# Kernel optimization log

Measured on AMD Instinct MI355X. Metric: run time of the kernel, lower is better.

## Reference

```python
import jax, jax.numpy as jnp
import numpy as np

B, L, K, H = 2, 2048, 48, 128
NUM_IN = 2 * H          # h_E (H) + gathered h_V (H)
SCALE = 30.0            # EncLayer scale
LN_EPS = 1e-5


def _linear_params(key, fan_in, fan_out):
    kw, kb = jax.random.split(key)
    s = 1.0 / np.sqrt(fan_in)
    W = jax.random.uniform(kw, (fan_in, fan_out), minval=-s, maxval=s, dtype=jnp.float32)
    b = jax.random.uniform(kb, (fan_out,), minval=-s, maxval=s, dtype=jnp.float32)
    return W, b


def setup_inputs() -> dict:
    key = jax.random.key(0)
    ks = jax.random.split(key, 12)
    h_V = jax.random.normal(ks[0], (B, L, H), dtype=jnp.float32)
    h_E = jax.random.normal(ks[1], (B, L, K, H), dtype=jnp.float32)
    E_idx = jax.random.randint(ks[2], (B, L, K), 0, L, dtype=jnp.int64)
    mask_V = jnp.ones((B, L), dtype=jnp.float32)
    mask_attend = jnp.ones((B, L, K), dtype=jnp.float32)

    W1, b1 = _linear_params(ks[3], H + NUM_IN, H)
    W2, b2 = _linear_params(ks[4], H, H)
    W3, b3 = _linear_params(ks[5], H, H)
    W11, b11 = _linear_params(ks[6], H + NUM_IN, H)
    W12, b12 = _linear_params(ks[7], H, H)
    W13, b13 = _linear_params(ks[8], H, H)
    Wi, bi = _linear_params(ks[9], H, 4 * H)   # PositionWiseFeedForward W_in
    Wo, bo = _linear_params(ks[10], 4 * H, H)  # W_out

    ln = lambda: (jnp.ones((H,), jnp.float32), jnp.zeros((H,), jnp.float32))
    ln1_s, ln1_b = ln(); ln2_s, ln2_b = ln(); ln3_s, ln3_b = ln()

    return dict(h_V=h_V, h_E=h_E, E_idx=E_idx, mask_V=mask_V, mask_attend=mask_attend,
                W1=W1, b1=b1, W2=W2, b2=b2, W3=W3, b3=b3,
                W11=W11, b11=b11, W12=W12, b12=b12, W13=W13, b13=b13,
                Wi=Wi, bi=bi, Wo=Wo, bo=bo,
                ln1_s=ln1_s, ln1_b=ln1_b, ln2_s=ln2_s, ln2_b=ln2_b,
                ln3_s=ln3_s, ln3_b=ln3_b)


def gather_nodes(nodes, idx):
    # nodes: [B, L, H], idx: [B, L, K] -> [B, L, K, H]
    b, l, h = nodes.shape
    flat = idx.reshape(b, -1)  # [B, L*K]
    g = jnp.take_along_axis(nodes, flat[..., None], axis=1)  # [B, L*K, H]
    return g.reshape(b, idx.shape[1], idx.shape[2], h)


def layer_norm(x, scale, bias):
    mu = jnp.mean(x, axis=-1, keepdims=True)
    var = jnp.mean((x - mu) ** 2, axis=-1, keepdims=True)
    return (x - mu) / jnp.sqrt(var + LN_EPS) * scale + bias


def gelu(x):
    return jax.nn.gelu(x, approximate=False)  # torch nn.GELU default (erf)


def enc_layer_forward(h_V, h_E, E_idx, mask_V, mask_attend, p):
    # --- node update: gather neighbors, concat, MLP, masked sum-reduce ---
    h_EV = jnp.concatenate([h_E, gather_nodes(h_V, E_idx)], axis=-1)        # [B,L,K,2H]
    h_V_exp = jnp.broadcast_to(h_V[:, :, None, :], h_EV.shape[:3] + (h_V.shape[-1],))
    h_EV = jnp.concatenate([h_V_exp, h_EV], axis=-1)                        # [B,L,K,3H]
    m = gelu(h_EV @ p['W1'] + p['b1'])
    m = gelu(m @ p['W2'] + p['b2'])
    m = m @ p['W3'] + p['b3']
    m = mask_attend[..., None] * m
    dh = jnp.sum(m, axis=-2) / SCALE                                        # [B,L,H]
    h_V = layer_norm(h_V + dh, p['ln1_s'], p['ln1_b'])
    # --- position-wise FFN ---
    dh = gelu(h_V @ p['Wi'] + p['bi']) @ p['Wo'] + p['bo']
    h_V = layer_norm(h_V + dh, p['ln2_s'], p['ln2_b'])
    h_V = mask_V[..., None] * h_V
    # --- edge update ---
    h_EV = jnp.concatenate([h_E, gather_nodes(h_V, E_idx)], axis=-1)
    h_V_exp = jnp.broadcast_to(h_V[:, :, None, :], h_EV.shape[:3] + (h_V.shape[-1],))
    h_EV = jnp.concatenate([h_V_exp, h_EV], axis=-1)
    m = gelu(h_EV @ p['W11'] + p['b11'])
    m = gelu(m @ p['W12'] + p['b12'])
    m = m @ p['W13'] + p['b13']
    h_E = layer_norm(h_E + m, p['ln3_s'], p['ln3_b'])
    return h_V, h_E


def reference(h_V, h_E, E_idx, mask_V, mask_attend,
              W1, b1, W2, b2, W3, b3, W11, b11, W12, b12, W13, b13,
              Wi, bi, Wo, bo, ln1_s, ln1_b, ln2_s, ln2_b, ln3_s, ln3_b):
    p = dict(W1=W1, b1=b1, W2=W2, b2=b2, W3=W3, b3=b3,
             W11=W11, b11=b11, W12=W12, b12=b12, W13=W13, b13=b13,
             Wi=Wi, bi=bi, Wo=Wo, bo=bo,
             ln1_s=ln1_s, ln1_b=ln1_b, ln2_s=ln2_s, ln2_b=ln2_b,
             ln3_s=ln3_s, ln3_b=ln3_b)
    return enc_layer_forward(h_V, h_E, E_idx, mask_V, mask_attend, p)
```

## Files before the change

kernel.cpp:

```cpp
#include <hip/hip_runtime.h>
#include <hip/hip_bf16.h>
#include <math.h>

typedef unsigned short u16;
typedef __attribute__((ext_vector_type(8))) short bf16x8;
typedef __attribute__((ext_vector_type(4))) float f32x4;
typedef __attribute__((ext_vector_type(4))) unsigned int uint4v;
typedef __attribute__((ext_vector_type(2))) unsigned int uint2v;
typedef __attribute__((ext_vector_type(4))) unsigned short u16x4;

#define BB 2
#define LL 2048
#define KN 48
#define HH 128
#define NBLK (BB*LL)
#define ST 136

#define WOFF      16
#define OFF_W1MT  (WOFF + 0)
#define OFF_W1ST  (WOFF + 16384)
#define OFF_W1GT  (WOFF + 32768)
#define OFF_W2T   (WOFF + 49152)
#define OFF_W3T   (WOFF + 65536)
#define OFF_W11MT (WOFF + 81920)
#define OFF_W11ST (WOFF + 98304)
#define OFF_W11GT (WOFF + 114688)
#define OFF_W12T  (WOFF + 131072)
#define OFF_W13T  (WOFF + 147456)
#define OFF_WIT   (WOFF + 163840)
#define OFF_WOT   (WOFF + 229376)
#define OFF_HV1   (WOFF + 294912)
#define OFF_Q1    (WOFF + 819200)
#define OFF_Q2    (WOFF + 1343488)
#define OFF_R1    (WOFF + 1867776)
#define OFF_R2    (WOFF + 2916352)
#define PREP_N    294912

__device__ __forceinline__ float b2f(u16 u){
    union { unsigned int i; float f; } v; v.i = ((unsigned int)u) << 16; return v.f;
}
__device__ __forceinline__ u16 f2b(float f){
    unsigned int x = __float_as_uint(f);
    unsigned int r = x + 0x7fffu + ((x >> 16) & 1u);
    return (u16)(r >> 16);
}
__device__ __forceinline__ unsigned int f2b2(float lo, float hi){
    unsigned int r;
    asm("v_cvt_pk_bf16_f32 %0, %1, %2" : "=v"(r) : "v"(lo), "v"(hi));
    return r;
}
__device__ __forceinline__ float gelu_f(float x){
    float ax = fabsf(x) * 0.70710678118654752f;
    float t  = __builtin_amdgcn_rcpf(fmaf(0.3275911f, ax, 1.0f));
    float e  = __builtin_amdgcn_exp2f(ax * ax * -1.4426950408889634f);
    float p  = fmaf(1.061405429f, t, -1.453152027f);
    p = fmaf(p, t, 1.421413741f);
    p = fmaf(p, t, -0.284496736f);
    p = fmaf(p, t, 0.254829592f);
    p = p * t;
    float erfv = fmaf(-p, e, 1.0f);
    float hx = 0.5f * x;
    return fmaf(fabsf(hx), erfv, hx);
}
__device__ __forceinline__ u16 ldb(const void* p, long i, int f32){
    return f32 ? f2b(((const float*)p)[i]) : ((const u16*)p)[i];
}
__device__ __forceinline__ float ldf(const void* p, long i, int f32){
    return f32 ? ((const float*)p)[i] : b2f(((const u16*)p)[i]);
}
__device__ __forceinline__ f32x4 ldf4(const void* p, long i, int f32){
    f32x4 r;
    if (f32){
        r = *(const f32x4*)((const float*)p + i);
    } else {
        u16x4 v = *(const u16x4*)((const u16*)p + i);
        r[0]=b2f(v[0]); r[1]=b2f(v[1]); r[2]=b2f(v[2]); r[3]=b2f(v[3]);
    }
    return r;
}
__device__ __forceinline__ void st4(void* p, long i, f32x4 v, int f32){
    if (f32){
        *(f32x4*)((float*)p + i) = v;
    } else {
        uint2v u; u.x = f2b2(v[0], v[1]); u.y = f2b2(v[2], v[3]);
        *(uint2v*)((u16*)p + i) = u;
    }
}
__device__ __forceinline__ void stage8(u16* dst, const void* src, long off, int f32){
    if (f32){
        const float* s = (const float*)src + off;
        f32x4 a = *(const f32x4*)(s);
        f32x4 b = *(const f32x4*)(s + 4);
        uint4v v;
        v.x = f2b2(a[0], a[1]); v.y = f2b2(a[2], a[3]);
        v.z = f2b2(b[0], b[1]); v.w = f2b2(b[2], b[3]);
        *(uint4v*)dst = v;
    } else {
        *(uint4v*)dst = *(const uint4v*)((const u16*)src + off);
    }
}
__device__ __forceinline__ int ld_idx(const void* p, int i, int i64){
    int v = i64 ? ((const int*)p)[2*i] : ((const int*)p)[i];
    return v & (LL - 1);
}

__global__ void prep_kernel(const void* W1, const void* W2, const void* W3,
                            const void* W11, const void* W12, const void* W13,
                            const void* Wi, const void* Wo,
                            const void* ln1s, const void* maskV, const void* eidx,
                            u16* wsbase){
    unsigned l0 = ((const unsigned*)ln1s)[0];
    unsigned m0 = ((const unsigned*)maskV)[0];
    const int f32 = (l0 == 0x3F800000u || m0 == 0x3F800000u) ? 1 : 0;
    if (blockIdx.x == 0 && threadIdx.x == 0){
        const int* e = (const int*)eidx;
        int orodd = 0, orlow = 0;
        for (int i = 1; i < 64; i += 2) orodd |= e[i];
        for (int i = 0; i < 64; i += 2) orlow |= e[i];
        ((int*)wsbase)[0] = f32;
        ((int*)wsbase)[1] = (orodd == 0 && orlow != 0) ? 1 : 0;
    }
    int i = blockIdx.x * 256 + threadIdx.x;
    if (i < 16384){ int n = i >> 7, k = i & 127; wsbase[OFF_W1MT + i] = ldb(W1, (128 + k)*128 + n, f32); }
    else if (i < 32768){ int j = i - 16384;  int n = j >> 7, k = j & 127; wsbase[OFF_W1ST  + j] = ldb(W1, k*128 + n, f32); }
    else if (i < 49152){ int j = i - 32768;  int n = j >> 7, k = j & 127; wsbase[OFF_W1GT  + j] = ldb(W1, (256 + k)*128 + n, f32); }
    else if (i < 65536){ int j = i - 49152;  int n = j >> 7, k = j & 127; wsbase[OFF_W2T   + j] = ldb(W2, k*128 + n, f32); }
    else if (i < 81920){ int j = i - 65536;  int n = j >> 7, k = j & 127; wsbase[OFF_W3T   + j] = ldb(W3, k*128 + n, f32); }
    else if (i < 98304){ int j = i - 81920;  int n = j >> 7, k = j & 127; wsbase[OFF_W11MT + j] = ldb(W11, (128 + k)*128 + n, f32); }
    else if (i < 114688){ int j = i - 98304; int n = j >> 7, k = j & 127; wsbase[OFF_W11ST + j] = ldb(W11, k*128 + n, f32); }
    else if (i < 131072){ int j = i - 114688;int n = j >> 7, k = j & 127; wsbase[OFF_W11GT + j] = ldb(W11, (256 + k)*128 + n, f32); }
    else if (i < 147456){ int j = i - 131072;int n = j >> 7, k = j & 127; wsbase[OFF_W12T  + j] = ldb(W12, k*128 + n, f32); }
    else if (i < 163840){ int j = i - 147456;int n = j >> 7, k = j & 127; wsbase[OFF_W13T  + j] = ldb(W13, k*128 + n, f32); }
    else if (i < 229376){ int j = i - 163840; int h = j >> 7, c = j & 127; wsbase[OFF_WIT + j] = ldb(Wi, c*512 + h, f32); }
    else if (i < 294912){ int j = i - 229376; int c = j >> 9, h = j & 511; wsbase[OFF_WOT + j] = ldb(Wo, h*128 + c, f32); }
}

__global__ __launch_bounds__(256) void precomp_kernel(
    const void* __restrict__ src, const void* __restrict__ bias,
    u16* __restrict__ wsbase, long offWs, long offWg, long offQ, long offR)
{
    __shared__ alignas(16) u16 X[16 * ST];
    const int f32 = ((const int*)wsbase)[0];
    const int t = threadIdx.x, lane = t & 63, w = t >> 6;
    const int node0 = blockIdx.x * 16;
    const int r16 = lane & 15, q = lane >> 4, q8 = q * 8;

    {
        int row = t >> 4, ch = t & 15;
        stage8(X + row * ST + ch * 8, src, ((long)(node0 + row)) * HH + ch * 8, f32);
    }
    __syncthreads();

    const u16* bp = X + r16 * ST + q8;
#pragma unroll
    for (int half = 0; half < 2; half++){
        long offW = half ? offWg : offWs;
#pragma unroll
        for (int nt = 0; nt < 2; nt++){
            int wr = w * 32 + nt * 16 + r16;
            const u16* ap = wsbase + offW + (long)wr * 128 + q8;
            f32x4 acc; acc[0]=0.f; acc[1]=0.f; acc[2]=0.f; acc[3]=0.f;
#pragma unroll
            for (int kk = 0; kk < 4; kk++){
                bf16x8 av = *(const bf16x8*)(ap + kk * 32);
                bf16x8 bv = *(const bf16x8*)(bp + kk * 32);
                acc = __builtin_amdgcn_mfma_f32_16x16x32_bf16(av, bv, acc, 0, 0, 0);
            }
            int c0 = w * 32 + nt * 16 + q * 4;
            if (half == 0){
                f32x4 bc = ldf4(bias, c0, f32);
                float* Rf = (float*)(wsbase + offR);
                f32x4 rr; rr[0]=acc[0]+bc[0]; rr[1]=acc[1]+bc[1]; rr[2]=acc[2]+bc[2]; rr[3]=acc[3]+bc[3];
                *(f32x4*)(Rf + (long)(node0 + r16) * HH + c0) = rr;
            } else {
                uint2v u; u.x = f2b2(acc[0], acc[1]); u.y = f2b2(acc[2], acc[3]);
                *(uint2v*)(wsbase + offQ + (long)(node0 + r16) * HH + c0) = u;
            }
        }
    }
}

__device__ __forceinline__ void mfma_WB(const u16* Mls, const bf16x8* W,
                                        f32x4 acc[3], int lane){
    const int r16 = lane & 15;
    const int q8  = (lane >> 4) * 8;
    const u16* bp = Mls + r16 * ST + q8;
#pragma unroll
    for (int kk = 0; kk < 4; kk++){
        bf16x8 b0 = *(const bf16x8*)(bp + kk * 32);
        bf16x8 b1 = *(const bf16x8*)(bp + 16 * ST + kk * 32);
        bf16x8 b2 = *(const bf16x8*)(bp + 32 * ST + kk * 32);
        acc[0] = __builtin_amdgcn_mfma_f32_16x16x32_bf16(W[kk], b0, acc[0], 0, 0, 0);
        acc[1] = __builtin_amdgcn_mfma_f32_16x16x32_bf16(W[kk], b1, acc[1], 0, 0, 0);
        acc[2] = __builtin_amdgcn_mfma_f32_16x16x32_bf16(W[kk], b2, acc[2], 0, 0, 0);
    }
}

__device__ __forceinline__ void zero_acc3(f32x4 acc[3]){
#pragma unroll
    for (int m = 0; m < 3; m++){ acc[m][0]=0.f; acc[m][1]=0.f; acc[m][2]=0.f; acc[m][3]=0.f; }
}

__device__ __forceinline__ void init_accT(f32x4 acc[3], const u16* Qg, int lane, int w){
    const int r16 = lane & 15, q = lane >> 4;
    const int c0 = w * 16 + q * 4;
#pragma unroll
    for (int mt = 0; mt < 3; mt++){
        u16x4 v = *(const u16x4*)(Qg + (mt * 16 + r16) * ST + c0);
        acc[mt][0]=b2f(v[0]); acc[mt][1]=b2f(v[1]); acc[mt][2]=b2f(v[2]); acc[mt][3]=b2f(v[3]);
    }
}

__device__ __forceinline__ void store_T(f32x4 acc[3], u16* M, f32x4 bc4,
                                        int lane, int w, bool dogelu){
    const int r16 = lane & 15, q = lane >> 4;
    const int c0 = w * 16 + q * 4;
#pragma unroll
    for (int mt = 0; mt < 3; mt++){
        float v0 = acc[mt][0] + bc4[0], v1 = acc[mt][1] + bc4[1];
        float v2 = acc[mt][2] + bc4[2], v3 = acc[mt][3] + bc4[3];
        if (dogelu){ v0 = gelu_f(v0); v1 = gelu_f(v1); v2 = gelu_f(v2); v3 = gelu_f(v3); }
        uint2v u; u.x = f2b2(v0, v1); u.y = f2b2(v2, v3);
        *(uint2v*)(M + (mt * 16 + r16) * ST + c0) = u;
    }
}

__global__ __launch_bounds__(512, 6) void node_kernel(
    const void* __restrict__ hV, const void* __restrict__ hE, const void* __restrict__ Eidx,
    const void* __restrict__ maskA,
    const void* __restrict__ b2, const void* __restrict__ b3,
    const void* __restrict__ ln1s, const void* __restrict__ ln1b,
    u16* __restrict__ wsbase)
{
    __shared__ alignas(16) u16 A[KN * ST];
    __shared__ alignas(16) u16 Qg[KN * ST];
    __shared__ float smask[KN];
    __shared__ alignas(16) float sL[HH];
    __shared__ alignas(16) float dh[HH];
    __shared__ float hv0f[HH];
    u16* M1 = Qg;

    const int f32 = ((const int*)wsbase)[0];
    const int i64 = ((const int*)wsbase)[1];
    const u16* ws = wsbase;
    const int t = threadIdx.x, lane = t & 63, w = t >> 6;
    const int bid = blockIdx.x;
    const int b = bid >> 11;
    const int r16 = lane & 15, q = lane >> 4, q8 = q * 8;
    const int wrow = w * 16 + r16;
    const int c0 = w * 16 + q * 4;

    bf16x8 B1[4];
    {
        const u16* bp = ws + OFF_W1MT + (long)wrow * 128 + q8;
#pragma unroll
        for (int k = 0; k < 4; k++) B1[k] = *(const bf16x8*)(bp + k * 32);
    }

    for (int i = t; i < 768; i += 512){
        int row = i >> 4, ch = i & 15;
        stage8(A + row * ST + ch * 8, hE, ((long)bid * KN + row) * HH + ch * 8, f32);
    }
    for (int i = t; i < 768; i += 512){
        int row = i >> 4, ch = i & 15;
        int nb = ld_idx(Eidx, bid * KN + row, i64);
        *(uint4v*)(Qg + row * ST + ch * 8) =
            *(const uint4v*)(ws + OFF_Q1 + ((long)b * LL + nb) * HH + ch * 8);
    }
    if (t < HH) hv0f[t] = ldf(hV, (long)bid * HH + t, f32);
    if (t < KN) smask[t] = ldf(maskA, bid * KN + t, f32);

    bf16x8 B2[4];
    {
        const u16* bp = ws + OFF_W2T + (long)wrow * 128 + q8;
#pragma unroll
        for (int k = 0; k < 4; k++) B2[k] = *(const bf16x8*)(bp + k * 32);
    }
    const f32x4 bc1 = *(const f32x4*)((const float*)(wsbase + OFF_R1) + (long)bid * HH + c0);
    __syncthreads();

    f32x4 acc[3];
    init_accT(acc, Qg, lane, w);
    __builtin_amdgcn_s_setprio(1);
    mfma_WB(A, B1, acc, lane);
    __builtin_amdgcn_s_setprio(0);
    store_T(acc, M1, bc1, lane, w, true);
    __syncthreads();

    zero_acc3(acc);
    __builtin_amdgcn_s_setprio(1);
    mfma_WB(M1, B2, acc, lane);
    __builtin_amdgcn_s_setprio(0);

    float cnt;
    {
        f32x4 b2v = ldf4(b2, c0, f32);
        f32x4 s; s[0]=0.f; s[1]=0.f; s[2]=0.f; s[3]=0.f;
        float cm = smask[r16] + smask[16 + r16] + smask[32 + r16];
#pragma unroll
        for (int mt = 0; mt < 3; mt++){
            float mk = smask[mt * 16 + r16];
#pragma unroll
            for (int j = 0; j < 4; j++)
                s[j] += mk * gelu_f(acc[mt][j] + b2v[j]);
        }
#pragma unroll
        for (int off = 1; off <= 8; off <<= 1){
#pragma unroll
            for (int j = 0; j < 4; j++) s[j] += __shfl_xor(s[j], off);
            cm += __shfl_xor(cm, off);
        }
        cnt = cm;
        if (r16 == 0) *(f32x4*)&sL[c0] = s;
    }
    __syncthreads();

    {
        int n = t >> 2, p = t & 3;
        const u16* wr = ws + OFF_W3T + (long)n * 128 + p * 32;
        float a = 0.f;
#pragma unroll
        for (int cc = 0; cc < 8; cc++){
            u16x4 wv = *(const u16x4*)(wr + cc * 4);
            f32x4 sv = *(const f32x4*)&sL[p * 32 + cc * 4];
            a = fmaf(b2f(wv[0]), sv[0], a);
            a = fmaf(b2f(wv[1]), sv[1], a);
            a = fmaf(b2f(wv[2]), sv[2], a);
            a = fmaf(b2f(wv[3]), sv[3], a);
        }
        a += __shfl_xor(a, 1);
        a += __shfl_xor(a, 2);
        if (p == 0) dh[n] = a + cnt * ldf(b3, n, f32);
    }
    __syncthreads();

    if (w == 0){
        float xa = hv0f[lane]      + dh[lane]      * (1.0f / 30.0f);
        float xb = hv0f[64 + lane] + dh[64 + lane] * (1.0f / 30.0f);
        float sum = xa + xb, sq = xa * xa + xb * xb;
#pragma unroll
        for (int off = 1; off < 64; off <<= 1){ sum += __shfl_xor(sum, off); sq += __shfl_xor(sq, off); }
        float mu = sum * (1.0f / 128.0f);
        float var = sq * (1.0f / 128.0f) - mu * mu;
        float rstd = rsqrtf(var + 1e-5f);
        wsbase[OFF_HV1 + (long)bid * HH + lane] =
            f2b((xa - mu) * rstd * ldf(ln1s, lane, f32) + ldf(ln1b, lane, f32));
        wsbase[OFF_HV1 + (long)bid * HH + 64 + lane] =
            f2b((xb - mu) * rstd * ldf(ln1s, 64 + lane, f32) + ldf(ln1b, 64 + lane, f32));
    }
}

__global__ __launch_bounds__(512, 6) void ffn_kernel(
    const void* __restrict__ maskV,
    const void* __restrict__ bi, const void* __restrict__ bo,
    const void* __restrict__ b11,
    const void* __restrict__ ln2s, const void* __restrict__ ln2b,
    u16* __restrict__ wsbase, void* __restrict__ dout)
{
    __shared__ alignas(16) u16 X[16 * 136];
    __shared__ alignas(16) u16 Hid[16 * 520];
    __shared__ alignas(16) float V[16 * 132];

    const int f32 = ((const int*)wsbase)[0];
    const u16* ws = wsbase;
    const u16* hv1 = wsbase + OFF_HV1;
    const int t = threadIdx.x, lane = t & 63, w = t >> 6;
    const int node0 = blockIdx.x * 16;
    const int r16 = lane & 15, q = lane >> 4, q8 = q * 8;
    const int c0 = w * 16 + q * 4;

    if (t < 256){
        int row = t >> 4, ch = t & 15;
        *(uint4v*)(X + row * 136 + ch * 8) =
            *(const uint4v*)(hv1 + (long)(node0 + row) * HH + ch * 8);
    }
    __syncthreads();

    f32x4 acc[4];
#pragma unroll
    for (int nt = 0; nt < 4; nt++){ acc[nt][0]=0.f; acc[nt][1]=0.f; acc[nt][2]=0.f; acc[nt][3]=0.f; }
    {
        const u16* bp = X + r16 * 136 + q8;
#pragma unroll
        for (int kk = 0; kk < 4; kk++){
            bf16x8 bv = *(const bf16x8*)(bp + kk * 32);
#pragma unroll
            for (int nt = 0; nt < 4; nt++){
                const u16* ap = ws + OFF_WIT + (long)(w * 64 + nt * 16 + r16) * 128 + kk * 32 + q8;
                bf16x8 av = *(const bf16x8*)ap;
                acc[nt] = __builtin_amdgcn_mfma_f32_16x16x32_bf16(av, bv, acc[nt], 0, 0, 0);
            }
        }
    }
#pragma unroll
    for (int nt = 0; nt < 4; nt++){
        int hc0 = w * 64 + nt * 16 + q * 4;
        f32x4 bc = ldf4(bi, hc0, f32);
        float g0 = gelu_f(acc[nt][0] + bc[0]), g1 = gelu_f(acc[nt][1] + bc[1]);
        float g2 = gelu_f(acc[nt][2] + bc[2]), g3 = gelu_f(acc[nt][3] + bc[3]);
        uint2v u; u.x = f2b2(g0, g1); u.y = f2b2(g2, g3);
        *(uint2v*)(Hid + r16 * 520 + hc0) = u;
    }
    __syncthreads();

    f32x4 acc2; acc2[0]=0.f; acc2[1]=0.f; acc2[2]=0.f; acc2[3]=0.f;
    {
        const u16* ap = ws + OFF_WOT + (long)(w * 16 + r16) * 512 + q8;
        const u16* bp = Hid + r16 * 520 + q8;
        __builtin_amdgcn_s_setprio(1);
#pragma unroll
        for (int kk = 0; kk < 16; kk++){
            bf16x8 av = *(const bf16x8*)(ap + kk * 32);
            bf16x8 bv = *(const bf16x8*)(bp + kk * 32);
            acc2 = __builtin_amdgcn_mfma_f32_16x16x32_bf16(av, bv, acc2, 0, 0, 0);
        }
        __builtin_amdgcn_s_setprio(0);
    }
    {
        f32x4 bo4 = ldf4(bo, c0, f32);
        u16x4 xr = *(const u16x4*)(X + r16 * 136 + c0);
        f32x4 vv;
        vv[0] = acc2[0] + bo4[0] + b2f(xr[0]);
        vv[1] = acc2[1] + bo4[1] + b2f(xr[1]);
        vv[2] = acc2[2] + bo4[2] + b2f(xr[2]);
        vv[3] = acc2[3] + bo4[3] + b2f(xr[3]);
        *(f32x4*)&V[r16 * 132 + c0] = vv;
    }
    __syncthreads();

    {
        int row = t >> 5, p = t & 31;
        f32x4 v = *(const f32x4*)&V[row * 132 + p * 4];
        float sum = v[0] + v[1] + v[2] + v[3];
        float sq = v[0]*v[0] + v[1]*v[1] + v[2]*v[2] + v[3]*v[3];
#pragma unroll
        for (int off = 1; off < 32; off <<= 1){ sum += __shfl_xor(sum, off); sq += __shfl_xor(sq, off); }
        float mu = sum * (1.0f / 128.0f);
        float var = sq * (1.0f / 128.0f) - mu * mu;
        float rstd = rsqrtf(var + 1e-5f);
        float mv = ldf(maskV, node0 + row, f32);
        f32x4 s4 = ldf4(ln2s, p * 4, f32), bb4 = ldf4(ln2b, p * 4, f32);
        f32x4 y;
#pragma unroll
        for (int j = 0; j < 4; j++) y[j] = ((v[j] - mu) * rstd * s4[j] + bb4[j]) * mv;
        st4(dout, (long)(node0 + row) * HH + p * 4, y, f32);
        uint2v u; u.x = f2b2(y[0], y[1]); u.y = f2b2(y[2], y[3]);
        *(uint2v*)(X + row * 136 + p * 4) = u;
    }
    __syncthreads();

    {
        const u16* bp = X + r16 * 136 + q8;
        f32x4 aR, aQ;
        aR[0]=0.f; aR[1]=0.f; aR[2]=0.f; aR[3]=0.f;
        aQ[0]=0.f; aQ[1]=0.f; aQ[2]=0.f; aQ[3]=0.f;
#pragma unroll
        for (int kk = 0; kk < 4; kk++){
            bf16x8 bv = *(const bf16x8*)(bp + kk * 32);
            bf16x8 avR = *(const bf16x8*)(ws + OFF_W11ST + (long)(w * 16 + r16) * 128 + kk * 32 + q8);
            bf16x8 avQ = *(const bf16x8*)(ws + OFF_W11GT + (long)(w * 16 + r16) * 128 + kk * 32 + q8);
            aR = __builtin_amdgcn_mfma_f32_16x16x32_bf16(avR, bv, aR, 0, 0, 0);
            aQ = __builtin_amdgcn_mfma_f32_16x16x32_bf16(avQ, bv, aQ, 0, 0, 0);
        }
        f32x4 b11v = ldf4(b11, c0, f32);
        float* Rf = (float*)(wsbase + OFF_R2);
        f32x4 rr;
#pragma unroll
        for (int j = 0; j < 4; j++) rr[j] = aR[j] + b11v[j];
        *(f32x4*)(Rf + (long)(node0 + r16) * HH + c0) = rr;
        uint2v u; u.x = f2b2(aQ[0], aQ[1]); u.y = f2b2(aQ[2], aQ[3]);
        *(uint2v*)(wsbase + OFF_Q2 + (long)(node0 + r16) * HH + c0) = u;
    }
}

__global__ __launch_bounds__(512, 6) void edge_kernel(
    const void* __restrict__ hE, const void* __restrict__ Eidx,
    const void* __restrict__ b12, const void* __restrict__ b13,
    const void* __restrict__ ln3s, const void* __restrict__ ln3b,
    u16* __restrict__ wsbase, void* __restrict__ dout)
{
    __shared__ alignas(16) u16 A[KN * ST];
    __shared__ alignas(16) u16 Qg[KN * ST];
    __shared__ float rowsum[KN];
    __shared__ float rowsq[KN];
    u16* M1 = Qg;
    u16* M2 = A;

    const int f32 = ((const int*)wsbase)[0];
    const int i64 = ((const int*)wsbase)[1];
    const u16* ws = wsbase;
    const int t = threadIdx.x, lane = t & 63, w = t >> 6;
    const int bid = blockIdx.x;
    const int b = bid >> 11;
    const int r16 = lane & 15, q = lane >> 4, q8 = q * 8;
    const int wrow = w * 16 + r16;
    const int c0 = w * 16 + q * 4;

    bf16x8 B1[4];
    {
        const u16* bp = ws + OFF_W11MT + (long)wrow * 128 + q8;
#pragma unroll
        for (int k = 0; k < 4; k++) B1[k] = *(const bf16x8*)(bp + k * 32);
    }

    for (int i = t; i < 768; i += 512){
        int row = i >> 4, ch = i & 15;
        stage8(A + row * ST + ch * 8, hE, ((long)bid * KN + row) * HH + ch * 8, f32);
    }
    for (int i = t; i < 768; i += 512){
        int row = i >> 4, ch = i & 15;
        int nb = ld_idx(Eidx, bid * KN + row, i64);
        *(uint4v*)(Qg + row * ST + ch * 8) =
            *(const uint4v*)(ws + OFF_Q2 + ((long)b * LL + nb) * HH + ch * 8);
    }
    if (t < KN){ rowsum[t] = 0.f; rowsq[t] = 0.f; }

    bf16x8 B2[4];
    {
        const u16* bp = ws + OFF_W12T + (long)wrow * 128 + q8;
#pragma unroll
        for (int k = 0; k < 4; k++) B2[k] = *(const bf16x8*)(bp + k * 32);
    }
    const f32x4 bc1 = *(const f32x4*)((const float*)(wsbase + OFF_R2) + (long)bid * HH + c0);
    __syncthreads();

    f32x4 acc[3];
    init_accT(acc, Qg, lane, w);
    __builtin_amdgcn_s_setprio(1);
    mfma_WB(A, B1, acc, lane);
    __builtin_amdgcn_s_setprio(0);
    store_T(acc, M1, bc1, lane, w, true);

    bf16x8 B3[4];
    {
        const u16* bp = ws + OFF_W13T + (long)wrow * 128 + q8;
#pragma unroll
        for (int k = 0; k < 4; k++) B3[k] = *(const bf16x8*)(bp + k * 32);
    }
    __syncthreads();

    zero_acc3(acc);
    __builtin_amdgcn_s_setprio(1);
    mfma_WB(M1, B2, acc, lane);
    __builtin_amdgcn_s_setprio(0);
    store_T(acc, M2, ldf4(b12, c0, f32), lane, w, true);
    __syncthreads();

    zero_acc3(acc);
    __builtin_amdgcn_s_setprio(1);
    mfma_WB(M2, B3, acc, lane);
    __builtin_amdgcn_s_setprio(0);

    f32x4 vals[3];
    {
        f32x4 b13v = ldf4(b13, c0, f32);
#pragma unroll
        for (int mt = 0; mt < 3; mt++){
            int r = mt * 16 + r16;
            f32x4 res = ldf4(hE, ((long)bid * KN + r) * HH + c0, f32);
#pragma unroll
            for (int j = 0; j < 4; j++) vals[mt][j] = acc[mt][j] + b13v[j] + res[j];
        }
    }
    {
        float s[3], ss[3];
#pragma unroll
        for (int mt = 0; mt < 3; mt++){
            s[mt]  = vals[mt][0] + vals[mt][1] + vals[mt][2] + vals[mt][3];
            ss[mt] = vals[mt][0]*vals[mt][0] + vals[mt][1]*vals[mt][1]
                   + vals[mt][2]*vals[mt][2] + vals[mt][3]*vals[mt][3];
            s[mt]  += __shfl_xor(s[mt], 16);  s[mt]  += __shfl_xor(s[mt], 32);
            ss[mt] += __shfl_xor(ss[mt], 16); ss[mt] += __shfl_xor(ss[mt], 32);
        }
        if (lane < 16){
#pragma unroll
            for (int mt = 0; mt < 3; mt++){
                atomicAdd(&rowsum[mt * 16 + lane], s[mt]);
                atomicAdd(&rowsq[mt * 16 + lane], ss[mt]);
            }
        }
    }
    __syncthreads();
    if (t < KN){
        float mu = rowsum[t] * (1.0f / 128.0f);
        float var = rowsq[t] * (1.0f / 128.0f) - mu * mu;
        rowsum[t] = mu;
        rowsq[t] = rsqrtf(var + 1e-5f);
    }
    __syncthreads();

    {
        long ebase = (long)BB * LL * HH;
        f32x4 g4 = ldf4(ln3s, c0, f32), be4 = ldf4(ln3b, c0, f32);
#pragma unroll
        for (int mt = 0; mt < 3; mt++){
            int r = mt * 16 + r16;
            float mu = rowsum[r], rs = rowsq[r];
            f32x4 y;
#pragma unroll
            for (int j = 0; j < 4; j++) y[j] = (vals[mt][j] - mu) * rs * g4[j] + be4[j];
            st4(dout, ebase + ((long)bid * KN + r) * HH + c0, y, f32);
        }
    }
}

extern "C" void kernel_launch(void* const* d_in, const int* in_sizes, int n_in,
                              void* d_out, int out_size, void* d_ws, size_t ws_size,
                              hipStream_t stream) {
    const void* hV    = d_in[0];
    const void* hE    = d_in[1];
    const void* Eidx  = d_in[2];
    const void* maskV = d_in[3];
    const void* maskA = d_in[4];
    const void* W1  = d_in[5];  const void* b1  = d_in[6];
    const void* W2  = d_in[7];  const void* b2  = d_in[8];
    const void* W3  = d_in[9];  const void* b3  = d_in[10];
    const void* W11 = d_in[11]; const void* b11 = d_in[12];
    const void* W12 = d_in[13]; const void* b12 = d_in[14];
    const void* W13 = d_in[15]; const void* b13 = d_in[16];
    const void* Wi  = d_in[17]; const void* bi  = d_in[18];
    const void* Wo  = d_in[19]; const void* bo  = d_in[20];
    const void* ln1s = d_in[21]; const void* ln1b = d_in[22];
    const void* ln2s = d_in[23]; const void* ln2b = d_in[24];
    const void* ln3s = d_in[25]; const void* ln3b = d_in[26];

    u16* ws = (u16*)d_ws;

    prep_kernel<<<(PREP_N + 255) / 256, 256, 0, stream>>>(W1, W2, W3, W11, W12, W13, Wi, Wo,
                                                          ln1s, maskV, Eidx, ws);
    precomp_kernel<<<NBLK / 16, 256, 0, stream>>>(hV, b1, ws,
                                                  (long)OFF_W1ST, (long)OFF_W1GT,
                                                  (long)OFF_Q1, (long)OFF_R1);
    node_kernel<<<NBLK, 512, 0, stream>>>(hV, hE, Eidx, maskA,
                                          b2, b3, ln1s, ln1b, ws);
    ffn_kernel<<<NBLK / 16, 512, 0, stream>>>(maskV, bi, bo, b11, ln2s, ln2b, ws, d_out);
    edge_kernel<<<NBLK, 512, 0, stream>>>(hE, Eidx, b12, b13,
                                          ln3s, ln3b, ws, d_out);
}
```

Before: 370.3 us.

## Process two nodes per block with register-prefetched next-node staging

Node and edge kernels now handle two consecutive nodes per block, launching half as many blocks. While the first node's MFMA chain runs, the second node's h_E tile and gathered Q rows are loaded into registers and written to a spare LDS buffer between barriers. This hides global load latency and amortizes the weight-fragment loads over two nodes. The cost is more LDS per block (an extra 48x136 tile), more live registers, and fewer blocks to fill the GPU, which may lower occupancy.

Result: slower. 576.8 us (+55.8%).

```diff
diff --git a/kernel.cpp b/kernel.cpp
--- a/kernel.cpp
+++ b/kernel.cpp
@@ -232,121 +232,168 @@
     const void* __restrict__ ln1s, const void* __restrict__ ln1b,
     u16* __restrict__ wsbase)
 {
-    __shared__ alignas(16) u16 A[KN * ST];
-    __shared__ alignas(16) u16 Qg[KN * ST];
-    __shared__ float smask[KN];
+    __shared__ alignas(16) u16 A0[KN * ST];
+    __shared__ alignas(16) u16 A1[KN * ST];
+    __shared__ alignas(16) u16 G[KN * ST];
+    __shared__ float smask2[2 * KN];
     __shared__ alignas(16) float sL[HH];
     __shared__ alignas(16) float dh[HH];
-    __shared__ float hv0f[HH];
-    u16* M1 = Qg;
+    __shared__ float hv0f2[2 * HH];
 
     const int f32 = ((const int*)wsbase)[0];
     const int i64 = ((const int*)wsbase)[1];
     const u16* ws = wsbase;
     const int t = threadIdx.x, lane = t & 63, w = t >> 6;
-    const int bid = blockIdx.x;
-    const int b = bid >> 11;
+    const int bid0 = blockIdx.x * 2;
     const int r16 = lane & 15, q = lane >> 4, q8 = q * 8;
     const int wrow = w * 16 + r16;
     const int c0 = w * 16 + q * 4;
 
-    bf16x8 B1[4];
+    bf16x8 B1[4], B2[4];
     {
         const u16* bp = ws + OFF_W1MT + (long)wrow * 128 + q8;
 #pragma unroll
         for (int k = 0; k < 4; k++) B1[k] = *(const bf16x8*)(bp + k * 32);
+        bp = ws + OFF_W2T + (long)wrow * 128 + q8;
+#pragma unroll
+        for (int k = 0; k < 4; k++) B2[k] = *(const bf16x8*)(bp + k * 32);
     }
 
     for (int i = t; i < 768; i += 512){
         int row = i >> 4, ch = i & 15;
-        stage8(A + row * ST + ch * 8, hE, ((long)bid * KN + row) * HH + ch * 8, f32);
-    }
-    for (int i = t; i < 768; i += 512){
-        int row = i >> 4, ch = i & 15;
-        int nb = ld_idx(Eidx, bid * KN + row, i64);
-        *(uint4v*)(Qg + row * ST + ch * 8) =
-            *(const uint4v*)(ws + OFF_Q1 + ((long)b * LL + nb) * HH + ch * 8);
-    }
-    if (t < HH) hv0f[t] = ldf(hV, (long)bid * HH + t, f32);
-    if (t < KN) smask[t] = ldf(maskA, bid * KN + t, f32);
-
-    bf16x8 B2[4];
-    {
-        const u16* bp = ws + OFF_W2T + (long)wrow * 128 + q8;
-#pragma unroll
-        for (int k = 0; k < 4; k++) B2[k] = *(const bf16x8*)(bp + k * 32);
-    }
-    const f32x4 bc1 = *(const f32x4*)((const float*)(wsbase + OFF_R1) + (long)bid * HH + c0);
+        stage8(A0 + row * ST + ch * 8, hE, ((long)bid0 * KN + row) * HH + ch * 8, f32);
+    }
+    {
+        const int b0 = bid0 >> 11;
+        for (int i = t; i < 768; i += 512){
+            int row = i >> 4, ch = i & 15;
+            int nb = ld_idx(Eidx, bid0 * KN + row, i64);
+            *(uint4v*)(G + row * ST + ch * 8) =
+                *(const uint4v*)(ws + OFF_Q1 + ((long)b0 * LL + nb) * HH + ch * 8);
+        }
+    }
+    if (t < 2 * HH) hv0f2[t] = ldf(hV, (long)bid0 * HH + t, f32);
+    if (t >= 416) smask2[t - 416] = ldf(maskA, (long)bid0 * KN + (t - 416), f32);
     __syncthreads();
 
-    f32x4 acc[3];
-    init_accT(acc, Qg, lane, w);
-    __builtin_amdgcn_s_setprio(1);
-    mfma_WB(A, B1, acc, lane);
-    __builtin_amdgcn_s_setprio(0);
-    store_T(acc, M1, bc1, lane, w, true);
-    __syncthreads();
-
-    zero_acc3(acc);
-    __builtin_amdgcn_s_setprio(1);
-    mfma_WB(M1, B2, acc, lane);
-    __builtin_amdgcn_s_setprio(0);
-
-    float cnt;
-    {
-        f32x4 b2v = ldf4(b2, c0, f32);
-        f32x4 s; s[0]=0.f; s[1]=0.f; s[2]=0.f; s[3]=0.f;
-        float cm = smask[r16] + smask[16 + r16] + smask[32 + r16];
-#pragma unroll
-        for (int mt = 0; mt < 3; mt++){
-            float mk = smask[mt * 16 + r16];
-#pragma unroll
-            for (int j = 0; j < 4; j++)
-                s[j] += mk * gelu_f(acc[mt][j] + b2v[j]);
-        }
-#pragma unroll
-        for (int off = 1; off <= 8; off <<= 1){
-#pragma unroll
-            for (int j = 0; j < 4; j++) s[j] += __shfl_xor(s[j], off);
-            cm += __shfl_xor(cm, off);
-        }
-        cnt = cm;
-        if (r16 == 0) *(f32x4*)&sL[c0] = s;
-    }
-    __syncthreads();
-
-    {
-        int n = t >> 2, p = t & 3;
-        const u16* wr = ws + OFF_W3T + (long)n * 128 + p * 32;
-        float a = 0.f;
-#pragma unroll
-        for (int cc = 0; cc < 8; cc++){
-            u16x4 wv = *(const u16x4*)(wr + cc * 4);
-            f32x4 sv = *(const f32x4*)&sL[p * 32 + cc * 4];
-            a = fmaf(b2f(wv[0]), sv[0], a);
-            a = fmaf(b2f(wv[1]), sv[1], a);
-            a = fmaf(b2f(wv[2]), sv[2], a);
-            a = fmaf(b2f(wv[3]), sv[3], a);
-        }
-        a += __shfl_xor(a, 1);
-        a += __shfl_xor(a, 2);
-        if (p == 0) dh[n] = a + cnt * ldf(b3, n, f32);
-    }
-    __syncthreads();
-
-    if (w == 0){
-        float xa = hv0f[lane]      + dh[lane]      * (1.0f / 30.0f);
-        float xb = hv0f[64 + lane] + dh[64 + lane] * (1.0f / 30.0f);
-        float sum = xa + xb, sq = xa * xa + xb * xb;
-#pragma unroll
-        for (int off = 1; off < 64; off <<= 1){ sum += __shfl_xor(sum, off); sq += __shfl_xor(sq, off); }
-        float mu = sum * (1.0f / 128.0f);
-        float var = sq * (1.0f / 128.0f) - mu * mu;
-        float rstd = rsqrtf(var + 1e-5f);
-        wsbase[OFF_HV1 + (long)bid * HH + lane] =
-            f2b((xa - mu) * rstd * ldf(ln1s, lane, f32) + ldf(ln1b, lane, f32));
-        wsbase[OFF_HV1 + (long)bid * HH + 64 + lane] =
-            f2b((xb - mu) * rstd * ldf(ln1s, 64 + lane, f32) + ldf(ln1b, 64 + lane, f32));
+    f32x4 hf0, hf1, hf2; uint4v hb0, hb1, qg0, qg1;
+
+    for (int j = 0; j < 2; ++j){
+        const int n = bid0 + j;
+        u16* Ac = j ? A1 : A0;
+        u16* An = j ? A0 : A1;
+        const f32x4 bc1 = *(const f32x4*)((const float*)(wsbase + OFF_R1) + (long)n * HH + c0);
+
+        if (j == 0){
+            const int n1 = bid0 + 1;
+            const int bn1 = n1 >> 11;
+            if (f32){
+                const float* s = (const float*)hE + (long)n1 * KN * HH;
+                hf0 = *(const f32x4*)(s + t * 4);
+                hf1 = *(const f32x4*)(s + (t + 512) * 4);
+                hf2 = *(const f32x4*)(s + (t + 1024) * 4);
+            } else {
+                const u16* s = (const u16*)hE + (long)n1 * KN * HH;
+                hb0 = *(const uint4v*)(s + t * 8);
+                if (t < 256) hb1 = *(const uint4v*)(s + (t + 512) * 8);
+            }
+            {
+                int nb = ld_idx(Eidx, n1 * KN + (t >> 4), i64);
+                qg0 = *(const uint4v*)(ws + OFF_Q1 + ((long)bn1 * LL + nb) * HH + (t & 15) * 8);
+                if (t < 256){
+                    int nb1 = ld_idx(Eidx, n1 * KN + ((512 + t) >> 4), i64);
+                    qg1 = *(const uint4v*)(ws + OFF_Q1 + ((long)bn1 * LL + nb1) * HH + ((512 + t) & 15) * 8);
+                }
+            }
+        }
+
+        f32x4 acc[3];
+        init_accT(acc, G, lane, w);
+        __builtin_amdgcn_s_setprio(1);
+        mfma_WB(Ac, B1, acc, lane);
+        __builtin_amdgcn_s_setprio(0);
+        store_T(acc, G, bc1, lane, w, true);
+        __syncthreads();
+
+        zero_acc3(acc);
+        __builtin_amdgcn_s_setprio(1);
+        mfma_WB(G, B2, acc, lane);
+        __builtin_amdgcn_s_setprio(0);
+
+        float cnt;
+        {
+            f32x4 b2v = ldf4(b2, c0, f32);
+            f32x4 s; s[0]=0.f; s[1]=0.f; s[2]=0.f; s[3]=0.f;
+            float cm = smask2[j*KN + r16] + smask2[j*KN + 16 + r16] + smask2[j*KN + 32 + r16];
+#pragma unroll
+            for (int mt = 0; mt < 3; mt++){
+                float mk = smask2[j*KN + mt * 16 + r16];
+#pragma unroll
+                for (int jj = 0; jj < 4; jj++)
+                    s[jj] += mk * gelu_f(acc[mt][jj] + b2v[jj]);
+            }
+#pragma unroll
+            for (int off = 1; off <= 8; off <<= 1){
+#pragma unroll
+                for (int jj = 0; jj < 4; jj++) s[jj] += __shfl_xor(s[jj], off);
+                cm += __shfl_xor(cm, off);
+            }
+            cnt = cm;
+            if (r16 == 0) *(f32x4*)&sL[c0] = s;
+        }
+        if (j == 0){
+            if (f32){
+                uint2v u;
+                u.x = f2b2(hf0[0], hf0[1]); u.y = f2b2(hf0[2], hf0[3]);
+                *(uint2v*)(An + (t >> 5) * ST + (t & 31) * 4) = u;
+                u.x = f2b2(hf1[0], hf1[1]); u.y = f2b2(hf1[2], hf1[3]);
+                *(uint2v*)(An + ((t + 512) >> 5) * ST + ((t + 512) & 31) * 4) = u;
+                u.x = f2b2(hf2[0], hf2[1]); u.y = f2b2(hf2[2], hf2[3]);
+                *(uint2v*)(An + ((t + 1024) >> 5) * ST + ((t + 1024) & 31) * 4) = u;
+            } else {
+                *(uint4v*)(An + (t >> 4) * ST + (t & 15) * 8) = hb0;
+                if (t < 256) *(uint4v*)(An + ((t + 512) >> 4) * ST + ((t + 512) & 15) * 8) = hb1;
+            }
+        }
+        __syncthreads();
+
+        {
+            int nn = t >> 2, p = t & 3;
+            const u16* wr = ws + OFF_W3T + (long)nn * 128 + p * 32;
+            float a = 0.f;
+#pragma unroll
+            for (int cc = 0; cc < 8; cc++){
+                u16x4 wv = *(const u16x4*)(wr + cc * 4);
+                f32x4 sv = *(const f32x4*)&sL[p * 32 + cc * 4];
+                a = fmaf(b2f(wv[0]), sv[0], a);
+                a = fmaf(b2f(wv[1]), sv[1], a);
+                a = fmaf(b2f(wv[2]), sv[2], a);
+                a = fmaf(b2f(wv[3]), sv[3], a);
+            }
+            a += __shfl_xor(a, 1);
+            a += __shfl_xor(a, 2);
+            if (p == 0) dh[nn] = a + cnt * ldf(b3, nn, f32);
+        }
+        if (j == 0){
+            *(uint4v*)(G + (t >> 4) * ST + (t & 15) * 8) = qg0;
+            if (t < 256) *(uint4v*)(G + ((512 + t) >> 4) * ST + ((512 + t) & 15) * 8) = qg1;
+        }
+        __syncthreads();
+
+        if (w == 0){
+            float xa = hv0f2[j*HH + lane]      + dh[lane]      * (1.0f / 30.0f);
+            float xb = hv0f2[j*HH + 64 + lane] + dh[64 + lane] * (1.0f / 30.0f);
+            float sum = xa + xb, sq = xa * xa + xb * xb;
+#pragma unroll
+            for (int off = 1; off < 64; off <<= 1){ sum += __shfl_xor(sum, off); sq += __shfl_xor(sq, off); }
+            float mu = sum * (1.0f / 128.0f);
+            float var = sq * (1.0f / 128.0f) - mu * mu;
+            float rstd = rsqrtf(var + 1e-5f);
+            wsbase[OFF_HV1 + (long)n * HH + lane] =
+                f2b((xa - mu) * rstd * ldf(ln1s, lane, f32) + ldf(ln1b, lane, f32));
+            wsbase[OFF_HV1 + (long)n * HH + 64 + lane] =
+                f2b((xb - mu) * rstd * ldf(ln1s, 64 + lane, f32) + ldf(ln1b, 64 + lane, f32));
+        }
     }
 }
 
@@ -479,127 +526,168 @@
     const void* __restrict__ ln3s, const void* __restrict__ ln3b,
     u16* __restrict__ wsbase, void* __restrict__ dout)
 {
-    __shared__ alignas(16) u16 A[KN * ST];
-    __shared__ alignas(16) u16 Qg[KN * ST];
-    __shared__ float rowsum[KN];
-    __shared__ float rowsq[KN];
-    u16* M1 = Qg;
-    u16* M2 = A;
+    __shared__ alignas(16) u16 A0[KN * ST];
+    __shared__ alignas(16) u16 A1[KN * ST];
+    __shared__ alignas(16) u16 G[KN * ST];
+    __shared__ float rowsum[2 * KN];
+    __shared__ float rowsq[2 * KN];
 
     const int f32 = ((const int*)wsbase)[0];
     const int i64 = ((const int*)wsbase)[1];
     const u16* ws = wsbase;
     const int t = threadIdx.x, lane = t & 63, w = t >> 6;
-    const int bid = blockIdx.x;
-    const int b = bid >> 11;
+    const int bid0 = blockIdx.x * 2;
     const int r16 = lane & 15, q = lane >> 4, q8 = q * 8;
     const int wrow = w * 16 + r16;
     const int c0 = w * 16 + q * 4;
 
-    bf16x8 B1[4];
+    bf16x8 B1[4], B2[4], B3[4];
     {
         const u16* bp = ws + OFF_W11MT + (long)wrow * 128 + q8;
 #pragma unroll
         for (int k = 0; k < 4; k++) B1[k] = *(const bf16x8*)(bp + k * 32);
+        bp = ws + OFF_W12T + (long)wrow * 128 + q8;
+#pragma unroll
+        for (int k = 0; k < 4; k++) B2[k] = *(const bf16x8*)(bp + k * 32);
+        bp = ws + OFF_W13T + (long)wrow * 128 + q8;
+#pragma unroll
+        for (int k = 0; k < 4; k++) B3[k] = *(const bf16x8*)(bp + k * 32);
     }
 
     for (int i = t; i < 768; i += 512){
         int row = i >> 4, ch = i & 15;
-        stage8(A + row * ST + ch * 8, hE, ((long)bid * KN + row) * HH + ch * 8, f32);
-    }
-    for (int i = t; i < 768; i += 512){
-        int row = i >> 4, ch = i & 15;
-        int nb = ld_idx(Eidx, bid * KN + row, i64);
-        *(uint4v*)(Qg + row * ST + ch * 8) =
-            *(const uint4v*)(ws + OFF_Q2 + ((long)b * LL + nb) * HH + ch * 8);
-    }
-    if (t < KN){ rowsum[t] = 0.f; rowsq[t] = 0.f; }
-
-    bf16x8 B2[4];
-    {
-        const u16* bp = ws + OFF_W12T + (long)wrow * 128 + q8;
-#pragma unroll
-        for (int k = 0; k < 4; k++) B2[k] = *(const bf16x8*)(bp + k * 32);
-    }
-    const f32x4 bc1 = *(const f32x4*)((const float*)(wsbase + OFF_R2) + (long)bid * HH + c0);
+        stage8(A0 + row * ST + ch * 8, hE, ((long)bid0 * KN + row) * HH + ch * 8, f32);
+    }
+    {
+        const int b0 = bid0 >> 11;
+        for (int i = t; i < 768; i += 512){
+            int row = i >> 4, ch = i & 15;
+            int nb = ld_idx(Eidx, bid0 * KN + row, i64);
+            *(uint4v*)(G + row * ST + ch * 8) =
+                *(const uint4v*)(ws + OFF_Q2 + ((long)b0 * LL + nb) * HH + ch * 8);
+        }
+    }
+    if (t < 2 * KN){ rowsum[t] = 0.f; rowsq[t] = 0.f; }
     __syncthreads();
 
-    f32x4 acc[3];
-    init_accT(acc, Qg, lane, w);
-    __builtin_amdgcn_s_setprio(1);
-    mfma_WB(A, B1, acc, lane);
-    __builtin_amdgcn_s_setprio(0);
-    store_T(acc, M1, bc1, lane, w, true);
-
-    bf16x8 B3[4];
-    {
-        const u16* bp = ws + OFF_W13T + (long)wrow * 128 + q8;
-#pragma unroll
-        for (int k = 0; k < 4; k++) B3[k] = *(const bf16x8*)(bp + k * 32);
-    }
-    __syncthreads();
-
-    zero_acc3(acc);
-    __builtin_amdgcn_s_setprio(1);
-    mfma_WB(M1, B2, acc, lane);
-    __builtin_amdgcn_s_setprio(0);
-    store_T(acc, M2, ldf4(b12, c0, f32), lane, w, true);
-    __syncthreads();
-
-    zero_acc3(acc);
-    __builtin_amdgcn_s_setprio(1);
-    mfma_WB(M2, B3, acc, lane);
-    __builtin_amdgcn_s_setprio(0);
-
-    f32x4 vals[3];
-    {
-        f32x4 b13v = ldf4(b13, c0, f32);
-#pragma unroll
-        for (int mt = 0; mt < 3; mt++){
-            int r = mt * 16 + r16;
-            f32x4 res = ldf4(hE, ((long)bid * KN + r) * HH + c0, f32);
-#pragma unroll
-            for (int j = 0; j < 4; j++) vals[mt][j] = acc[mt][j] + b13v[j] + res[j];
-        }
-    }
-    {
-        float s[3], ss[3];
-#pragma unroll
-        for (int mt = 0; mt < 3; mt++){
-            s[mt]  = vals[mt][0] + vals[mt][1] + vals[mt][2] + vals[mt][3];
-            ss[mt] = vals[mt][0]*vals[mt][0] + vals[mt][1]*vals[mt][1]
-                   + vals[mt][2]*vals[mt][2] + vals[mt][3]*vals[mt][3];
-            s[mt]  += __shfl_xor(s[mt], 16);  s[mt]  += __shfl_xor(s[mt], 32);
-            ss[mt] += __shfl_xor(ss[mt], 16); ss[mt] += __shfl_xor(ss[mt], 32);
-        }
-        if (lane < 16){
+    f32x4 hf0, hf1, hf2; uint4v hb0, hb1, qg0, qg1;
+
+    for (int j = 0; j < 2; ++j){
+        const int n = bid0 + j;
+        u16* Ac = j ? A1 : A0;
+        u16* An = j ? A0 : A1;
+        const f32x4 bc1 = *(const f32x4*)((const float*)(wsbase + OFF_R2) + (long)n * HH + c0);
+
+        if (j == 0){
+            const int n1 = bid0 + 1;
+            const int bn1 = n1 >> 11;
+            if (f32){
+                const float* s = (const float*)hE + (long)n1 * KN * HH;
+                hf0 = *(const f32x4*)(s + t * 4);
+                hf1 = *(const f32x4*)(s + (t + 512) * 4);
+                hf2 = *(const f32x4*)(s + (t + 1024) * 4);
+            } else {
+                const u16* s = (const u16*)hE + (long)n1 * KN * HH;
+                hb0 = *(const uint4v*)(s + t * 8);
+                if (t < 256) hb1 = *(const uint4v*)(s + (t + 512) * 8);
+            }
+            {
+                int nb = ld_idx(Eidx, n1 * KN + (t >> 4), i64);
+                qg0 = *(const uint4v*)(ws + OFF_Q2 + ((long)bn1 * LL + nb) * HH + (t & 15) * 8);
+                if (t < 256){
+                    int nb1 = ld_idx(Eidx, n1 * KN + ((512 + t) >> 4), i64);
+                    qg1 = *(const uint4v*)(ws + OFF_Q2 + ((long)bn1 * LL + nb1) * HH + ((512 + t) & 15) * 8);
+                }
+            }
+        }
+
+        f32x4 acc[3];
+        init_accT(acc, G, lane, w);
+        __builtin_amdgcn_s_setprio(1);
+        mfma_WB(Ac, B1, acc, lane);
+        __builtin_amdgcn_s_setprio(0);
+        store_T(acc, G, bc1, lane, w, true);
+        __syncthreads();
+
+        zero_acc3(acc);
+        __builtin_amdgcn_s_setprio(1);
+        mfma_WB(G, B2, acc, lane);
+        __builtin_amdgcn_s_setprio(0);
+        store_T(acc, Ac, ldf4(b12, c0, f32), lane, w, true);
+        if (j == 0){
+            if (f32){
+                uint2v u;
+                u.x = f2b2(hf0[0], hf0[1]); u.y = f2b2(hf0[2], hf0[3]);
+                *(uint2v*)(An + (t >> 5) * ST + (t & 31) * 4) = u;
+                u.x = f2b2(hf1[0], hf1[1]); u.y = f2b2(hf1[2], hf1[3]);
+                *(uint2v*)(An + ((t + 512) >> 5) * ST + ((t + 512) & 31) * 4) = u;
+                u.x = f2b2(hf2[0], hf2[1]); u.y = f2b2(hf2[2], hf2[3]);
+                *(uint2v*)(An + ((t + 1024) >> 5) * ST + ((t + 1024) & 31) * 4) = u;
+            } else {
+                *(uint4v*)(An + (t >> 4) * ST + (t & 15) * 8) = hb0;
+                if (t < 256) *(uint4v*)(An + ((t + 512) >> 4) * ST + ((t + 512) & 15) * 8) = hb1;
+            }
+        }
+        __syncthreads();
+
+        zero_acc3(acc);
+        __builtin_amdgcn_s_setprio(1);
+        mfma_WB(Ac, B3, acc, lane);
+        __builtin_amdgcn_s_setprio(0);
+        if (j == 0){
+            *(uint4v*)(G + (t >> 4) * ST + (t & 15) * 8) = qg0;
+            if (t < 256) *(uint4v*)(G + ((512 + t) >> 4) * ST + ((512 + t) & 15) * 8) = qg1;
+        }
+
+        f32x4 vals[3];
+        {
+            f32x4 b13v = ldf4(b13, c0, f32);
 #pragma unroll
             for (int mt = 0; mt < 3; mt++){
-                atomicAdd(&rowsum[mt * 16 + lane], s[mt]);
-                atomicAdd(&rowsq[mt * 16 + lane], ss[mt]);
-            }
-        }
-    }
-    __syncthreads();
-    if (t < KN){
-        float mu = rowsum[t] * (1.0f / 128.0f);
-        float var = rowsq[t] * (1.0f / 128.0f) - mu * mu;
-        rowsum[t] = mu;
-        rowsq[t] = rsqrtf(var + 1e-5f);
-    }
-    __syncthreads();
-
-    {
-        long ebase = (long)BB * LL * HH;
-        f32x4 g4 = ldf4(ln3s, c0, f32), be4 = ldf4(ln3b, c0, f32);
-#pragma unroll
-        for (int mt = 0; mt < 3; mt++){
-            int r = mt * 16 + r16;
-            float mu = rowsum[r], rs = rowsq[r];
-            f32x4 y;
-#pragma unroll
-            for (int j = 0; j < 4; j++) y[j] = (vals[mt][j] - mu) * rs * g4[j] + be4[j];
-            st4(dout, ebase + ((long)bid * KN + r) * HH + c0, y, f32);
+                int r = mt * 16 + r16;
+                f32x4 res = ldf4(hE, ((long)n * KN + r) * HH + c0, f32);
+#pragma unroll
+                for (int jj = 0; jj < 4; jj++) vals[mt][jj] = acc[mt][jj] + b13v[jj] + res[jj];
+            }
+        }
+        {
+            float s[3], ss[3];
+#pragma unroll
+            for (int mt = 0; mt < 3; mt++){
+                s[mt]  = vals[mt][0] + vals[mt][1] + vals[mt][2] + vals[mt][3];
+                ss[mt] = vals[mt][0]*vals[mt][0] + vals[mt][1]*vals[mt][1]
+                       + vals[mt][2]*vals[mt][2] + vals[mt][3]*vals[mt][3];
+                s[mt]  += __shfl_xor(s[mt], 16);  s[mt]  += __shfl_xor(s[mt], 32);
+                ss[mt] += __shfl_xor(ss[mt], 16); ss[mt] += __shfl_xor(ss[mt], 32);
+            }
+            if (lane < 16){
+#pragma unroll
+                for (int mt = 0; mt < 3; mt++){
+                    atomicAdd(&rowsum[j*KN + mt * 16 + lane], s[mt]);
+                    atomicAdd(&rowsq[j*KN + mt * 16 + lane], ss[mt]);
+                }
+            }
+        }
+        __syncthreads();
+        if (t < KN){
+            float mu = rowsum[j*KN + t] * (1.0f / 128.0f);
+            float var = rowsq[j*KN + t] * (1.0f / 128.0f) - mu * mu;
+            rowsum[j*KN + t] = mu;
+            rowsq[j*KN + t] = rsqrtf(var + 1e-5f);
+        }
+        __syncthreads();
+        {
+            long ebase = (long)BB * LL * HH;
+            f32x4 g4 = ldf4(ln3s, c0, f32), be4 = ldf4(ln3b, c0, f32);
+#pragma unroll
+            for (int mt = 0; mt < 3; mt++){
+                int r = mt * 16 + r16;
+                float mu = rowsum[j*KN + r], rs = rowsq[j*KN + r];
+                f32x4 y;
+#pragma unroll
+                for (int jj = 0; jj < 4; jj++) y[jj] = (vals[mt][jj] - mu) * rs * g4[jj] + be4[jj];
+                st4(dout, ebase + ((long)n * KN + r) * HH + c0, y, f32);
+            }
         }
     }
 }
@@ -631,9 +719,9 @@
     precomp_kernel<<<NBLK / 16, 256, 0, stream>>>(hV, b1, ws,
                                                   (long)OFF_W1ST, (long)OFF_W1GT,
                                                   (long)OFF_Q1, (long)OFF_R1);
-    node_kernel<<<NBLK, 512, 0, stream>>>(hV, hE, Eidx, maskA,
-                                          b2, b3, ln1s, ln1b, ws);
+    node_kernel<<<NBLK / 2, 512, 0, stream>>>(hV, hE, Eidx, maskA,
+                                              b2, b3, ln1s, ln1b, ws);
     ffn_kernel<<<NBLK / 16, 512, 0, stream>>>(maskV, bi, bo, b11, ln2s, ln2b, ws, d_out);
-    edge_kernel<<<NBLK, 512, 0, stream>>>(hE, Eidx, b12, b13,
-                                          ln3s, ln3b, ws, d_out);
-}
+    edge_kernel<<<NBLK / 2, 512, 0, stream>>>(hE, Eidx, b12, b13,
+                                              ln3s, ln3b, ws, d_out);
+}
```
